# Kernel tuning notes

Hardware: AMD Instinct MI355X
Metric: run time of the kernel (lower is better)

## Reference

```python
import jax, jax.numpy as jnp
import numpy as np

B, T, K = 128, 1024, 24
START_TAG, END_TAG = 22, 23


def setup_inputs() -> dict:
    key = jax.random.key(0)
    k1, k2, k3 = jax.random.split(key, 3)
    scores = jax.random.normal(k1, (B, T, K, K), dtype=jnp.float32)
    targets = jax.random.randint(k2, (B, T), 0, K * K)
    # lengths must be sorted descending (pack_padded_sequence convention), >= 1
    lengths = jnp.sort(jax.random.randint(k3, (B,), 1, T + 1))[::-1]
    return {"scores": scores, "targets": targets, "lengths": lengths}


def reference(scores, targets, lengths):
    b, t_len, k, _ = scores.shape
    # gold path score: gather targets from flattened [B,T,K*K] view, mask by length
    flat = scores.reshape(b, t_len, k * k)
    scores_at_targets = jnp.take_along_axis(flat, targets[:, :, None], axis=2)[..., 0]  # [B,T]
    time_mask = jnp.arange(t_len)[None, :] < lengths[:, None]  # [B,T]
    gold_score = jnp.sum(jnp.where(time_mask, scores_at_targets, 0.0))

    # CRF forward recursion (log-sum-exp over previous tag), sequential over time.
    # t == 0: initialize with row of the <start> tag (all lengths >= 1).
    prev = scores[:, 0, START_TAG, :]  # [B,K]

    def step(prev, inp):
        s_t, m_t = inp  # s_t: [B,K,K], m_t: [B] bool (t < length)
        new = jax.scipy.special.logsumexp(s_t + prev[:, :, None], axis=1)  # [B,K]
        prev = jnp.where(m_t[:, None], new, prev)
        return prev, None

    s_rest = jnp.moveaxis(scores[:, 1:], 0, 1)  # time-major [T-1,B,K,K]
    m_rest = jnp.arange(1, t_len)[:, None] < lengths[None, :]  # [T-1,B]
    prev, _ = jax.lax.scan(step, prev, (s_rest, m_rest))

    all_paths_scores = prev[:, END_TAG].sum()
    return (all_paths_scores - gold_score) / b
```

## Files before the change

### kernel.cpp

```cpp
#include <hip/hip_runtime.h>

static constexpr int T_LEN = 1024;
static constexpr int KTAG = 24;
static constexpr int MAT = 576;
static constexpr int START_TAG = 22;
static constexpr int END_TAG = 23;
static constexpr int BATCH = 128;
static constexpr int CHUNK = 16;
static constexpr int NCHUNK = 64;

static constexpr float LOG2E = 1.4426950408889634f;
static constexpr float LN2   = 0.6931471805599453f;

typedef short  bf16x8 __attribute__((ext_vector_type(8)));
typedef float  f32x16 __attribute__((ext_vector_type(16)));

__device__ __forceinline__ float fexp2(float x) { return __builtin_amdgcn_exp2f(x); }
__device__ __forceinline__ float flog2(float x) { return __builtin_amdgcn_logf(x); }

__device__ __forceinline__ unsigned int f2bf(float x) {
  unsigned int u = __float_as_uint(x);
  u += 0x7FFFu + ((u >> 16) & 1u);
  return u >> 16;
}

__global__ __launch_bounds__(256) void chunkprod_kernel(
    const float* __restrict__ scores, const int* __restrict__ targets,
    const int* __restrict__ lengths,
    float* __restrict__ wsP, int* __restrict__ wsE, float* __restrict__ wsG)
{
  const int widx = threadIdx.x >> 6;
  const int lane = threadIdx.x & 63;
  const int i = blockIdx.x * 4 + widx;
  const int pr = i >> 1;
  const int anti = i & 1;
  const int b0i = pr >> 5;
  const int c0i = pr & 31;
  const int b = anti ? (127 - b0i) : b0i;
  const int c = anti ? (63 - c0i) : c0i;
  const int len = lengths[b];
  const int t0 = 1 + c * CHUNK;
  if (t0 >= len) return;
  const int n = min(CHUNK, len - t0);
  const int hd = lane >> 5;
  const int m = lane & 31;
  const int mc = m < KTAG ? m : KTAG - 1;
  const float* sb = scores + (size_t)b * T_LEN * MAT;

  {
    float gs = 0.f;
    if (lane < n) {
      int t = t0 + lane;
      gs = sb[(size_t)t * MAT + targets[b * T_LEN + t]];
    }
    #pragma unroll
    for (int off = 1; off < 64; off <<= 1) gs += __shfl_xor(gs, off, 64);
    if (lane == 0) wsG[b * NCHUNK + c] = gs;
  }

  int off1[8], off2[4];
  #pragma unroll
  for (int e = 0; e < 8; ++e) {
    int k = (e & 3) + 8 * (e >> 2) + 4 * hd;
    off1[e] = k * KTAG + mc;
  }
  #pragma unroll
  for (int e = 0; e < 4; ++e) {
    int k = 16 + e + 4 * hd;
    off2[e] = k * KTAG + mc;
  }

  float b0r[12], b1r[12], b2r[12], b3r[12];
  auto LOADA = [&](float (&buf)[12], int step) {
    const float* pb = sb + (size_t)(t0 + step) * MAT;
    #pragma unroll
    for (int e = 0; e < 8; ++e) buf[e] = pb[off1[e]];
    #pragma unroll
    for (int e = 0; e < 4; ++e) buf[8 + e] = pb[off2[e]];
  };

  unsigned int p[8];
  #pragma unroll
  for (int r = 0; r < 8; ++r) {
    int rlo = ((2 * r) & 3) + 8 * ((2 * r) >> 2) + 4 * hd;
    unsigned int v = 0;
    if (m == rlo)     v |= 0x3F80u;
    if (m == rlo + 1) v |= (0x3F80u << 16);
    p[r] = v;
  }

  int E = 0;

  auto STEPM = [&](const float (&buf)[12]) -> f32x16 {
    float av[12];
    #pragma unroll
    for (int q = 0; q < 12; ++q) av[q] = fexp2(buf[q] * LOG2E);
    bf16x8 a1, a2;
    #pragma unroll
    for (int e = 0; e < 8; ++e) a1[e] = (short)f2bf(av[e]);
    #pragma unroll
    for (int e = 0; e < 4; ++e) a2[e] = (short)f2bf(av[8 + e]);
    #pragma unroll
    for (int e = 4; e < 8; ++e) a2[e] = 0;
    union { unsigned int u[4]; bf16x8 v; } B1, B2;
    B1.u[0] = p[0]; B1.u[1] = p[1]; B1.u[2] = p[2]; B1.u[3] = p[3];
    B2.u[0] = p[4]; B2.u[1] = p[5]; B2.u[2] = p[6]; B2.u[3] = p[7];
    f32x16 d = {};
    d = __builtin_amdgcn_mfma_f32_32x32x16_bf16(a1, B1.v, d, 0, 0, 0);
    d = __builtin_amdgcn_mfma_f32_32x32x16_bf16(a2, B2.v, d, 0, 0, 0);
    return d;
  };

  auto CONV = [&](const f32x16& d) {
    int rb = __builtin_amdgcn_readfirstlane(__float_as_int(d[0]));
    int dd = ((rb >> 23) & 255) - 127;
    E += dd;
    float sc = __int_as_float((127 - dd) << 23);
    #pragma unroll
    for (int r = 0; r < 8; ++r)
      p[r] = (f2bf(d[2 * r + 1] * sc) << 16) | f2bf(d[2 * r] * sc);
  };

  LOADA(b0r, 0);
  LOADA(b1r, n > 1 ? 1 : 0);
  LOADA(b2r, n > 2 ? 2 : 0);
  LOADA(b3r, n > 3 ? 3 : 0);
  f32x16 z;
  int s = 0;
  for (;;) {
    z = STEPM(b0r);
    if (s + 1 >= n) break;
    CONV(z); { int t = s + 4; LOADA(b0r, t < n ? t : n - 1); }
    z = STEPM(b1r);
    if (s + 2 >= n) break;
    CONV(z); { int t = s + 5; LOADA(b1r, t < n ? t : n - 1); }
    z = STEPM(b2r);
    if (s + 3 >= n) break;
    CONV(z); { int t = s + 6; LOADA(b2r, t < n ? t : n - 1); }
    z = STEPM(b3r);
    if (s + 4 >= n) break;
    CONV(z); { int t = s + 7; LOADA(b3r, t < n ? t : n - 1); }
    s += 4;
  }

  if (m < KTAG) {
    float* dst = wsP + (size_t)(b * NCHUNK + c) * MAT + m * KTAG;
    *(float4*)(dst + 4 * hd)      = make_float4(z[0], z[1], z[2],  z[3]);
    *(float4*)(dst + 8 + 4 * hd)  = make_float4(z[4], z[5], z[6],  z[7]);
    *(float4*)(dst + 16 + 4 * hd) = make_float4(z[8], z[9], z[10], z[11]);
  }
  if (lane == 0) wsE[b * NCHUNK + c] = E;
}

__global__ __launch_bounds__(64) void chainmat_kernel(
    const float* __restrict__ scores, const int* __restrict__ targets,
    const float* __restrict__ wsP, const int* __restrict__ wsE,
    const float* __restrict__ wsG, const int* __restrict__ lengths,
    float* __restrict__ wsR)
{
  const int b = blockIdx.x;
  const int lane = threadIdx.x;
  const int hd = lane >> 5;
  const int m = lane & 31;
  const int mc = m < KTAG ? m : KTAG - 1;
  const int len = lengths[b];
  const int nc = (len + CHUNK - 2) >> 4;
  const float* sb = scores + (size_t)b * T_LEN * MAT;

  float gv = 0.f;
  if (lane < nc) gv = wsG[b * NCHUNK + lane];
  #pragma unroll
  for (int off = 1; off < 64; off <<= 1) gv += __shfl_xor(gv, off, 64);
  const float g0 = sb[targets[b * T_LEN]];

  if (nc == 0) {
    if (lane == 0) wsR[b] = sb[START_TAG * KTAG + END_TAG] - g0;
    return;
  }

  int ev = 0;
  if (lane < nc) ev = wsE[b * NCHUNK + lane];
  #pragma unroll
  for (int off = 1; off < 64; off <<= 1) ev += __shfl_xor(ev, off, 64);
  int E = ev;

  int off1[8], off2[4];
  #pragma unroll
  for (int e = 0; e < 8; ++e) {
    int k = (e & 3) + 8 * (e >> 2) + 4 * hd;
    off1[e] = k * KTAG + mc;
  }
  #pragma unroll
  for (int e = 0; e < 4; ++e) {
    int k = 16 + e + 4 * hd;
    off2[e] = k * KTAG + mc;
  }
  const float* pbase = wsP + (size_t)b * NCHUNK * MAT;

  float b0[12], b1[12];
  auto LOADP = [&](float (&buf)[12], int c) {
    const float* pb = pbase + (size_t)c * MAT;
    #pragma unroll
    for (int e = 0; e < 8; ++e) buf[e] = pb[off1[e]];
    #pragma unroll
    for (int e = 0; e < 4; ++e) buf[8 + e] = pb[off2[e]];
  };

  unsigned int p[8];
  #pragma unroll
  for (int r = 0; r < 8; ++r) {
    int rlo = ((2 * r) & 3) + 8 * ((2 * r) >> 2) + 4 * hd;
    unsigned int v = 0;
    if (m == rlo)     v |= 0x3F80u;
    if (m == rlo + 1) v |= (0x3F80u << 16);
    p[r] = v;
  }

  auto STEPP = [&](const float (&buf)[12]) -> f32x16 {
    bf16x8 a1, a2;
    #pragma unroll
    for (int e = 0; e < 8; ++e) a1[e] = (short)f2bf(buf[e]);
    #pragma unroll
    for (int e = 0; e < 4; ++e) a2[e] = (short)f2bf(buf[8 + e]);
    #pragma unroll
    for (int e = 4; e < 8; ++e) a2[e] = 0;
    union { unsigned int u[4]; bf16x8 v; } B1, B2;
    B1.u[0] = p[0]; B1.u[1] = p[1]; B1.u[2] = p[2]; B1.u[3] = p[3];
    B2.u[0] = p[4]; B2.u[1] = p[5]; B2.u[2] = p[6]; B2.u[3] = p[7];
    f32x16 d = {};
    d = __builtin_amdgcn_mfma_f32_32x32x16_bf16(a1, B1.v, d, 0, 0, 0);
    d = __builtin_amdgcn_mfma_f32_32x32x16_bf16(a2, B2.v, d, 0, 0, 0);
    return d;
  };
  auto CONVP = [&](const f32x16& d) {
    int rb = __builtin_amdgcn_readfirstlane(__float_as_int(d[0]));
    int dd = ((rb >> 23) & 255) - 127;
    E += dd;
    float sc = __int_as_float((127 - dd) << 23);
    #pragma unroll
    for (int r = 0; r < 8; ++r)
      p[r] = (f2bf(d[2 * r + 1] * sc) << 16) | f2bf(d[2 * r] * sc);
  };

  LOADP(b0, 0);
  LOADP(b1, nc > 1 ? 1 : 0);
  f32x16 z;
  int c = 0;
  for (;;) {
    z = STEPP(b0);
    if (c + 1 >= nc) break;
    CONVP(z); { int t = c + 2; LOADP(b0, t < nc ? t : nc - 1); }
    z = STEPP(b1);
    if (c + 2 >= nc) break;
    CONVP(z); { int t = c + 3; LOADP(b1, t < nc ? t : nc - 1); }
    c += 2;
  }

  float tau0 = fexp2(sb[START_TAG * KTAG + mc] * LOG2E);
  float v = (hd == 1 && m < KTAG) ? z[11] * tau0 : 0.f;
  #pragma unroll
  for (int off = 1; off < 64; off <<= 1) v += __shfl_xor(v, off, 64);
  if (lane == 0) {
    float logZ = ((float)E + flog2(v)) * LN2;
    wsR[b] = logZ - gv - g0;
  }
}

__global__ __launch_bounds__(64) void sum_kernel(
    const float* __restrict__ wsR, float* __restrict__ out)
{
  const int lane = threadIdx.x;
  float v = wsR[lane] + wsR[lane + 64];
  #pragma unroll
  for (int off = 1; off < 64; off <<= 1) v += __shfl_xor(v, off, 64);
  if (lane == 0) out[0] = v * (1.0f / (float)BATCH);
}

template<int DIR>
__device__ __forceinline__ int run_chain(const float* __restrict__ base, int len, int n,
                                         volatile float* __restrict__ tau,
                                         int lane, int h, int jj)
{
  int E = 0;
  float ref = 1.0f;
  float A[12], B[12], Cb[12];
  auto LOAD = [&](float (&buf)[12], int i) {
    if (DIR == 0) {
      const float* p = base + (size_t)(1 + i) * MAT + h * 12 * KTAG + jj;
      #pragma unroll
      for (int k = 0; k < 12; ++k) buf[k] = p[k * KTAG];
    } else {
      const float4* p = (const float4*)(base + (size_t)(len - 1 - i) * MAT + jj * KTAG + h * 12);
      float4 x = p[0], y = p[1], z = p[2];
      buf[0]=x.x; buf[1]=x.y; buf[2]=x.z; buf[3]=x.w;
      buf[4]=y.x; buf[5]=y.y; buf[6]=y.z; buf[7]=y.w;
      buf[8]=z.x; buf[9]=z.y; buf[10]=z.z; buf[11]=z.w;
    }
  };
  auto STEP = [&](const float (&buf)[12]) {
    int rb = __builtin_amdgcn_readfirstlane(__float_as_int(ref));
    int d = ((rb >> 23) & 255) - 127;
    float sc = __int_as_float((127 - d) << 23);
    E += d;
    float w[12];
    #pragma unroll
    for (int k = 0; k < 12; ++k) w[k] = fexp2(buf[k] * LOG2E);
    const float4* tp = (const float4*)((const float*)&tau[h * 12]);
    float4 t0 = tp[0], t1 = tp[1], t2 = tp[2];
    float a0 = t0.x*w[0], a1 = t0.y*w[1], a2 = t0.z*w[2], a3 = t0.w*w[3];
    a0 = fmaf(t1.x, w[4],  a0); a1 = fmaf(t1.y, w[5],  a1);
    a2 = fmaf(t1.z, w[6],  a2); a3 = fmaf(t1.w, w[7],  a3);
    a0 = fmaf(t2.x, w[8],  a0); a1 = fmaf(t2.y, w[9],  a1);
    a2 = fmaf(t2.z, w[10], a2); a3 = fmaf(t2.w, w[11], a3);
    float part = (a0 + a1) + (a2 + a3);
    float tot = part + __shfl_xor(part, 32, 64);
    float tn = tot * sc;
    if (lane < KTAG) tau[lane] = tn;
    ref = tn;
  };
  if (n > 0) {
    LOAD(A, 0); LOAD(B, n > 1 ? 1 : 0); LOAD(Cb, n > 2 ? 2 : 0);
    int i = 0;
    while (i + 3 <= n) {
      STEP(A);  { int ii = i + 3; LOAD(A,  ii < n ? ii : n - 1); }
      STEP(B);  { int ii = i + 4; LOAD(B,  ii < n ? ii : n - 1); }
      STEP(Cb); { int ii = i + 5; LOAD(Cb, ii < n ? ii : n - 1); }
      i += 3;
    }
    if (i < n)     STEP(A);
    if (i + 1 < n) STEP(B);
  }
  return E;
}

__global__ __launch_bounds__(128) void crf_fb_kernel(
    const float* __restrict__ scores, const int* __restrict__ lengths,
    float* __restrict__ acc)
{
  __shared__ float sm[2][32];
  __shared__ int smE[2];
  const int b = blockIdx.x;
  const int tid = threadIdx.x;
  const int wid = tid >> 6;
  const int lane = tid & 63;
  const int h = lane >> 5;
  const int j = lane & 31;
  const int jj = j < KTAG ? j : KTAG - 1;
  const int len = lengths[b];
  const float* base = scores + (size_t)b * T_LEN * MAT;
  const int m = len >> 1;
  volatile float* tau = sm[wid];
  int E;
  if (wid == 0) {
    if (lane < KTAG) tau[lane] = fexp2(base[START_TAG * KTAG + lane] * LOG2E);
    E = run_chain<0>(base, len, m, tau, lane, h, jj);
  } else {
    if (lane < KTAG) tau[lane] = (lane == END_TAG) ? 1.0f : 0.0f;
    E = run_chain<1>(base, len, len - 1 - m, tau, lane, h, jj);
  }
  if (lane == 0) smE[wid] = E;
  __syncthreads();
  if (wid == 0) {
    float v = (lane < KTAG) ? sm[0][lane] * sm[1][lane] : 0.0f;
    #pragma unroll
    for (int off = 1; off < 32; off <<= 1) v += __shfl_xor(v, off, 64);
    if (lane == 0) {
      float res = ((float)(smE[0] + smE[1]) + flog2(v)) * LN2;
      atomicAdd(acc, res);
    }
  }
}

__global__ __launch_bounds__(256) void gold_kernel(
    const float* __restrict__ scores, const int* __restrict__ targets,
    const int* __restrict__ lengths, float* __restrict__ acc)
{
  const int idx = blockIdx.x * blockDim.x + threadIdx.x;
  const int b = idx >> 10;
  const int t = idx & (T_LEN - 1);
  float v = 0.f;
  if (t < lengths[b]) v = scores[(size_t)idx * MAT + targets[idx]];
  #pragma unroll
  for (int off = 1; off < 64; off <<= 1) v += __shfl_xor(v, off, 64);
  if ((threadIdx.x & 63) == 0) atomicAdd(acc, -v);
}

__global__ void finalize_kernel(const float* __restrict__ acc, float* __restrict__ out) {
  out[0] = acc[0] * (1.0f / (float)BATCH);
}

extern "C" void kernel_launch(void* const* d_in, const int* in_sizes, int n_in,
                              void* d_out, int out_size, void* d_ws, size_t ws_size,
                              hipStream_t stream) {
  const float* scores = (const float*)d_in[0];
  const int* targets  = (const int*)d_in[1];
  const int* lengths  = (const int*)d_in[2];
  float* out = (float*)d_out;

  const size_t pbytes = (size_t)BATCH * NCHUNK * MAT * sizeof(float);
  const size_t ebytes = (size_t)BATCH * NCHUNK * sizeof(int);
  const size_t gbytes = (size_t)BATCH * NCHUNK * sizeof(float);
  const size_t need = pbytes + ebytes + gbytes + BATCH * sizeof(float);

  if (ws_size >= need) {
    float* wsP = (float*)d_ws;
    int*   wsE = (int*)((char*)d_ws + pbytes);
    float* wsG = (float*)((char*)d_ws + pbytes + ebytes);
    float* wsR = (float*)((char*)d_ws + pbytes + ebytes + gbytes);
    chunkprod_kernel<<<BATCH * NCHUNK / 4, 256, 0, stream>>>(scores, targets, lengths,
                                                             wsP, wsE, wsG);
    chainmat_kernel<<<BATCH, 64, 0, stream>>>(scores, targets, wsP, wsE, wsG,
                                              lengths, wsR);
    sum_kernel<<<1, 64, 0, stream>>>(wsR, out);
  } else {
    float* acc = (float*)d_ws;
    hipMemsetAsync(acc, 0, sizeof(float), stream);
    gold_kernel<<<BATCH * T_LEN / 256, 256, 0, stream>>>(scores, targets, lengths, acc);
    crf_fb_kernel<<<BATCH, 128, 0, stream>>>(scores, lengths, acc);
    finalize_kernel<<<1, 1, 0, stream>>>(acc, out);
  }
}
```

Measured before the change: 66.21 us.

## Stage score tiles via async global-to-LDS loads and double chunk length

After: 60.25 us. -9.0%, faster.

```diff
diff --git a/kernel.cpp b/kernel.cpp
--- a/kernel.cpp
+++ b/kernel.cpp
@@ -6,14 +6,17 @@
 static constexpr int START_TAG = 22;
 static constexpr int END_TAG = 23;
 static constexpr int BATCH = 128;
-static constexpr int CHUNK = 16;
-static constexpr int NCHUNK = 64;
+static constexpr int CHUNK = 32;
+static constexpr int NCHUNK = 32;
 
 static constexpr float LOG2E = 1.4426950408889634f;
 static constexpr float LN2   = 0.6931471805599453f;
 
 typedef short  bf16x8 __attribute__((ext_vector_type(8)));
 typedef float  f32x16 __attribute__((ext_vector_type(16)));
+
+typedef const __attribute__((address_space(1))) void* gas_t;
+typedef __attribute__((address_space(3))) void* las_t;
 
 __device__ __forceinline__ float fexp2(float x) { return __builtin_amdgcn_exp2f(x); }
 __device__ __forceinline__ float flog2(float x) { return __builtin_amdgcn_logf(x); }
@@ -29,15 +32,16 @@
     const int* __restrict__ lengths,
     float* __restrict__ wsP, int* __restrict__ wsE, float* __restrict__ wsG)
 {
+  __shared__ float stage[4][4][576];
   const int widx = threadIdx.x >> 6;
   const int lane = threadIdx.x & 63;
   const int i = blockIdx.x * 4 + widx;
   const int pr = i >> 1;
   const int anti = i & 1;
-  const int b0i = pr >> 5;
-  const int c0i = pr & 31;
+  const int b0i = pr >> 4;
+  const int c0i = pr & 15;
   const int b = anti ? (127 - b0i) : b0i;
-  const int c = anti ? (63 - c0i) : c0i;
+  const int c = anti ? (31 - c0i) : c0i;
   const int len = lengths[b];
   const int t0 = 1 + c * CHUNK;
   if (t0 >= len) return;
@@ -57,6 +61,7 @@
     for (int off = 1; off < 64; off <<= 1) gs += __shfl_xor(gs, off, 64);
     if (lane == 0) wsG[b * NCHUNK + c] = gs;
   }
+  asm volatile("s_waitcnt vmcnt(0)" ::: "memory");
 
   int off1[8], off2[4];
   #pragma unroll
@@ -70,13 +75,12 @@
     off2[e] = k * KTAG + mc;
   }
 
-  float b0r[12], b1r[12], b2r[12], b3r[12];
-  auto LOADA = [&](float (&buf)[12], int step) {
-    const float* pb = sb + (size_t)(t0 + step) * MAT;
-    #pragma unroll
-    for (int e = 0; e < 8; ++e) buf[e] = pb[off1[e]];
-    #pragma unroll
-    for (int e = 0; e < 4; ++e) buf[8 + e] = pb[off2[e]];
+  auto STAGE = [&](int slot, int t) {
+    const float* src = sb + (size_t)(t0 + t) * MAT;
+    float* dst = &stage[widx][slot][0];
+    __builtin_amdgcn_global_load_lds((gas_t)(src + lane * 4),       (las_t)dst,        16, 0, 0);
+    __builtin_amdgcn_global_load_lds((gas_t)(src + 256 + lane * 4), (las_t)(dst + 256),16, 0, 0);
+    __builtin_amdgcn_global_load_lds((gas_t)(src + 512 + lane),     (las_t)(dst + 512), 4, 0, 0);
   };
 
   unsigned int p[8];
@@ -121,26 +125,27 @@
       p[r] = (f2bf(d[2 * r + 1] * sc) << 16) | f2bf(d[2 * r] * sc);
   };
 
-  LOADA(b0r, 0);
-  LOADA(b1r, n > 1 ? 1 : 0);
-  LOADA(b2r, n > 2 ? 2 : 0);
-  LOADA(b3r, n > 3 ? 3 : 0);
+  STAGE(0, 0);
+  STAGE(1, n > 1 ? 1 : 0);
+  STAGE(2, n > 2 ? 2 : 0);
+  STAGE(3, n > 3 ? 3 : 0);
+
   f32x16 z;
   int s = 0;
   for (;;) {
-    z = STEPM(b0r);
+    asm volatile("s_waitcnt vmcnt(9)" ::: "memory");
+    const float* sl = &stage[widx][s & 3][0];
+    float raw[12];
+    #pragma unroll
+    for (int e = 0; e < 8; ++e) raw[e] = sl[off1[e]];
+    #pragma unroll
+    for (int e = 0; e < 4; ++e) raw[8 + e] = sl[off2[e]];
+    asm volatile("s_waitcnt lgkmcnt(0)" ::: "memory");
+    if (s + 1 < n) { int t = s + 4; STAGE(s & 3, t < n ? t : n - 1); }
+    z = STEPM(raw);
     if (s + 1 >= n) break;
-    CONV(z); { int t = s + 4; LOADA(b0r, t < n ? t : n - 1); }
-    z = STEPM(b1r);
-    if (s + 2 >= n) break;
-    CONV(z); { int t = s + 5; LOADA(b1r, t < n ? t : n - 1); }
-    z = STEPM(b2r);
-    if (s + 3 >= n) break;
-    CONV(z); { int t = s + 6; LOADA(b2r, t < n ? t : n - 1); }
-    z = STEPM(b3r);
-    if (s + 4 >= n) break;
-    CONV(z); { int t = s + 7; LOADA(b3r, t < n ? t : n - 1); }
-    s += 4;
+    CONV(z);
+    ++s;
   }
 
   if (m < KTAG) {
@@ -164,7 +169,7 @@
   const int m = lane & 31;
   const int mc = m < KTAG ? m : KTAG - 1;
   const int len = lengths[b];
-  const int nc = (len + CHUNK - 2) >> 4;
+  const int nc = (len + 30) >> 5;
   const float* sb = scores + (size_t)b * T_LEN * MAT;
 
   float gv = 0.f;
```

## Double chunk length, renormalize every other step, fuse final sum via atomic counter

Applied to the files above, without the earlier changes.

Result: faster. 61.79 us (-6.7%).

```diff
diff --git a/kernel.cpp b/kernel.cpp
--- a/kernel.cpp
+++ b/kernel.cpp
@@ -6,8 +6,8 @@
 static constexpr int START_TAG = 22;
 static constexpr int END_TAG = 23;
 static constexpr int BATCH = 128;
-static constexpr int CHUNK = 16;
-static constexpr int NCHUNK = 64;
+static constexpr int CHUNK = 32;
+static constexpr int NCHUNK = 32;
 
 static constexpr float LOG2E = 1.4426950408889634f;
 static constexpr float LN2   = 0.6931471805599453f;
@@ -34,10 +34,10 @@
   const int i = blockIdx.x * 4 + widx;
   const int pr = i >> 1;
   const int anti = i & 1;
-  const int b0i = pr >> 5;
-  const int c0i = pr & 31;
+  const int b0i = pr >> 4;
+  const int c0i = pr & 15;
   const int b = anti ? (127 - b0i) : b0i;
-  const int c = anti ? (63 - c0i) : c0i;
+  const int c = anti ? (31 - c0i) : c0i;
   const int len = lengths[b];
   const int t0 = 1 + c * CHUNK;
   if (t0 >= len) return;
@@ -111,7 +111,12 @@
     return d;
   };
 
-  auto CONV = [&](const f32x16& d) {
+  auto CONVL = [&](const f32x16& d) {
+    #pragma unroll
+    for (int r = 0; r < 8; ++r)
+      p[r] = (f2bf(d[2 * r + 1]) << 16) | f2bf(d[2 * r]);
+  };
+  auto CONVF = [&](const f32x16& d) {
     int rb = __builtin_amdgcn_readfirstlane(__float_as_int(d[0]));
     int dd = ((rb >> 23) & 255) - 127;
     E += dd;
@@ -130,16 +135,16 @@
   for (;;) {
     z = STEPM(b0r);
     if (s + 1 >= n) break;
-    CONV(z); { int t = s + 4; LOADA(b0r, t < n ? t : n - 1); }
+    CONVL(z); { int t = s + 4; LOADA(b0r, t < n ? t : n - 1); }
     z = STEPM(b1r);
     if (s + 2 >= n) break;
-    CONV(z); { int t = s + 5; LOADA(b1r, t < n ? t : n - 1); }
+    CONVF(z); { int t = s + 5; LOADA(b1r, t < n ? t : n - 1); }
     z = STEPM(b2r);
     if (s + 3 >= n) break;
-    CONV(z); { int t = s + 6; LOADA(b2r, t < n ? t : n - 1); }
+    CONVL(z); { int t = s + 6; LOADA(b2r, t < n ? t : n - 1); }
     z = STEPM(b3r);
     if (s + 4 >= n) break;
-    CONV(z); { int t = s + 7; LOADA(b3r, t < n ? t : n - 1); }
+    CONVF(z); { int t = s + 7; LOADA(b3r, t < n ? t : n - 1); }
     s += 4;
   }
 
@@ -156,7 +161,7 @@
     const float* __restrict__ scores, const int* __restrict__ targets,
     const float* __restrict__ wsP, const int* __restrict__ wsE,
     const float* __restrict__ wsG, const int* __restrict__ lengths,
-    float* __restrict__ wsR)
+    float* __restrict__ wsR, int* __restrict__ cnt, float* __restrict__ out)
 {
   const int b = blockIdx.x;
   const int lane = threadIdx.x;
@@ -164,112 +169,113 @@
   const int m = lane & 31;
   const int mc = m < KTAG ? m : KTAG - 1;
   const int len = lengths[b];
-  const int nc = (len + CHUNK - 2) >> 4;
+  const int nc = (len + 30) >> 5;
   const float* sb = scores + (size_t)b * T_LEN * MAT;
 
-  float gv = 0.f;
-  if (lane < nc) gv = wsG[b * NCHUNK + lane];
-  #pragma unroll
-  for (int off = 1; off < 64; off <<= 1) gv += __shfl_xor(gv, off, 64);
   const float g0 = sb[targets[b * T_LEN]];
 
   if (nc == 0) {
     if (lane == 0) wsR[b] = sb[START_TAG * KTAG + END_TAG] - g0;
-    return;
-  }
-
-  int ev = 0;
-  if (lane < nc) ev = wsE[b * NCHUNK + lane];
-  #pragma unroll
-  for (int off = 1; off < 64; off <<= 1) ev += __shfl_xor(ev, off, 64);
-  int E = ev;
-
-  int off1[8], off2[4];
-  #pragma unroll
-  for (int e = 0; e < 8; ++e) {
-    int k = (e & 3) + 8 * (e >> 2) + 4 * hd;
-    off1[e] = k * KTAG + mc;
-  }
-  #pragma unroll
-  for (int e = 0; e < 4; ++e) {
-    int k = 16 + e + 4 * hd;
-    off2[e] = k * KTAG + mc;
-  }
-  const float* pbase = wsP + (size_t)b * NCHUNK * MAT;
-
-  float b0[12], b1[12];
-  auto LOADP = [&](float (&buf)[12], int c) {
-    const float* pb = pbase + (size_t)c * MAT;
-    #pragma unroll
-    for (int e = 0; e < 8; ++e) buf[e] = pb[off1[e]];
-    #pragma unroll
-    for (int e = 0; e < 4; ++e) buf[8 + e] = pb[off2[e]];
-  };
-
-  unsigned int p[8];
-  #pragma unroll
-  for (int r = 0; r < 8; ++r) {
-    int rlo = ((2 * r) & 3) + 8 * ((2 * r) >> 2) + 4 * hd;
-    unsigned int v = 0;
-    if (m == rlo)     v |= 0x3F80u;
-    if (m == rlo + 1) v |= (0x3F80u << 16);
-    p[r] = v;
-  }
-
-  auto STEPP = [&](const float (&buf)[12]) -> f32x16 {
-    bf16x8 a1, a2;
-    #pragma unroll
-    for (int e = 0; e < 8; ++e) a1[e] = (short)f2bf(buf[e]);
-    #pragma unroll
-    for (int e = 0; e < 4; ++e) a2[e] = (short)f2bf(buf[8 + e]);
-    #pragma unroll
-    for (int e = 4; e < 8; ++e) a2[e] = 0;
-    union { unsigned int u[4]; bf16x8 v; } B1, B2;
-    B1.u[0] = p[0]; B1.u[1] = p[1]; B1.u[2] = p[2]; B1.u[3] = p[3];
-    B2.u[0] = p[4]; B2.u[1] = p[5]; B2.u[2] = p[6]; B2.u[3] = p[7];
-    f32x16 d = {};
-    d = __builtin_amdgcn_mfma_f32_32x32x16_bf16(a1, B1.v, d, 0, 0, 0);
-    d = __builtin_amdgcn_mfma_f32_32x32x16_bf16(a2, B2.v, d, 0, 0, 0);
-    return d;
-  };
-  auto CONVP = [&](const f32x16& d) {
-    int rb = __builtin_amdgcn_readfirstlane(__float_as_int(d[0]));
-    int dd = ((rb >> 23) & 255) - 127;
-    E += dd;
-    float sc = __int_as_float((127 - dd) << 23);
-    #pragma unroll
-    for (int r = 0; r < 8; ++r)
-      p[r] = (f2bf(d[2 * r + 1] * sc) << 16) | f2bf(d[2 * r] * sc);
-  };
-
-  LOADP(b0, 0);
-  LOADP(b1, nc > 1 ? 1 : 0);
-  f32x16 z;
-  int c = 0;
-  for (;;) {
-    z = STEPP(b0);
-    if (c + 1 >= nc) break;
-    CONVP(z); { int t = c + 2; LOADP(b0, t < nc ? t : nc - 1); }
-    z = STEPP(b1);
-    if (c + 2 >= nc) break;
-    CONVP(z); { int t = c + 3; LOADP(b1, t < nc ? t : nc - 1); }
-    c += 2;
-  }
-
-  float tau0 = fexp2(sb[START_TAG * KTAG + mc] * LOG2E);
-  float v = (hd == 1 && m < KTAG) ? z[11] * tau0 : 0.f;
-  #pragma unroll
-  for (int off = 1; off < 64; off <<= 1) v += __shfl_xor(v, off, 64);
-  if (lane == 0) {
-    float logZ = ((float)E + flog2(v)) * LN2;
-    wsR[b] = logZ - gv - g0;
-  }
-}
-
-__global__ __launch_bounds__(64) void sum_kernel(
-    const float* __restrict__ wsR, float* __restrict__ out)
-{
-  const int lane = threadIdx.x;
+  } else {
+    float gv = 0.f;
+    if (lane < nc) gv = wsG[b * NCHUNK + lane];
+    #pragma unroll
+    for (int off = 1; off < 64; off <<= 1) gv += __shfl_xor(gv, off, 64);
+
+    int ev = 0;
+    if (lane < nc) ev = wsE[b * NCHUNK + lane];
+    #pragma unroll
+    for (int off = 1; off < 64; off <<= 1) ev += __shfl_xor(ev, off, 64);
+    int E = ev;
+
+    int off1[8], off2[4];
+    #pragma unroll
+    for (int e = 0; e < 8; ++e) {
+      int k = (e & 3) + 8 * (e >> 2) + 4 * hd;
+      off1[e] = k * KTAG + mc;
+    }
+    #pragma unroll
+    for (int e = 0; e < 4; ++e) {
+      int k = 16 + e + 4 * hd;
+      off2[e] = k * KTAG + mc;
+    }
+    const float* pbase = wsP + (size_t)b * NCHUNK * MAT;
+
+    float f0[12], f1[12];
+    auto LOADP = [&](float (&buf)[12], int c) {
+      const float* pb = pbase + (size_t)c * MAT;
+      #pragma unroll
+      for (int e = 0; e < 8; ++e) buf[e] = pb[off1[e]];
+      #pragma unroll
+      for (int e = 0; e < 4; ++e) buf[8 + e] = pb[off2[e]];
+    };
+
+    unsigned int p[8];
+    #pragma unroll
+    for (int r = 0; r < 8; ++r) {
+      int rlo = ((2 * r) & 3) + 8 * ((2 * r) >> 2) + 4 * hd;
+      unsigned int v = 0;
+      if (m == rlo)     v |= 0x3F80u;
+      if (m == rlo + 1) v |= (0x3F80u << 16);
+      p[r] = v;
+    }
+
+    auto STEPP = [&](const float (&buf)[12]) -> f32x16 {
+      bf16x8 a1, a2;
+      #pragma unroll
+      for (int e = 0; e < 8; ++e) a1[e] = (short)f2bf(buf[e]);
+      #pragma unroll
+      for (int e = 0; e < 4; ++e) a2[e] = (short)f2bf(buf[8 + e]);
+      #pragma unroll
+      for (int e = 4; e < 8; ++e) a2[e] = 0;
+      union { unsigned int u[4]; bf16x8 v; } B1, B2;
+      B1.u[0] = p[0]; B1.u[1] = p[1]; B1.u[2] = p[2]; B1.u[3] = p[3];
+      B2.u[0] = p[4]; B2.u[1] = p[5]; B2.u[2] = p[6]; B2.u[3] = p[7];
+      f32x16 d = {};
+      d = __builtin_amdgcn_mfma_f32_32x32x16_bf16(a1, B1.v, d, 0, 0, 0);
+      d = __builtin_amdgcn_mfma_f32_32x32x16_bf16(a2, B2.v, d, 0, 0, 0);
+      return d;
+    };
+    auto CONVP = [&](const f32x16& d) {
+      int rb = __builtin_amdgcn_readfirstlane(__float_as_int(d[0]));
+      int dd = ((rb >> 23) & 255) - 127;
+      E += dd;
+      float sc = __int_as_float((127 - dd) << 23);
+      #pragma unroll
+      for (int r = 0; r < 8; ++r)
+        p[r] = (f2bf(d[2 * r + 1] * sc) << 16) | f2bf(d[2 * r] * sc);
+    };
+
+    LOADP(f0, 0);
+    LOADP(f1, nc > 1 ? 1 : 0);
+    f32x16 z;
+    int c = 0;
+    for (;;) {
+      z = STEPP(f0);
+      if (c + 1 >= nc) break;
+      CONVP(z); { int t = c + 2; LOADP(f0, t < nc ? t : nc - 1); }
+      z = STEPP(f1);
+      if (c + 2 >= nc) break;
+      CONVP(z); { int t = c + 3; LOADP(f1, t < nc ? t : nc - 1); }
+      c += 2;
+    }
+
+    float tau0 = fexp2(sb[START_TAG * KTAG + mc] * LOG2E);
+    float v = (hd == 1 && m < KTAG) ? z[11] * tau0 : 0.f;
+    #pragma unroll
+    for (int off = 1; off < 64; off <<= 1) v += __shfl_xor(v, off, 64);
+    if (lane == 0) {
+      float logZ = ((float)E + flog2(v)) * LN2;
+      wsR[b] = logZ - gv - g0;
+    }
+  }
+
+  __threadfence();
+  int old = 0;
+  if (lane == 0) old = atomicAdd(cnt, 1);
+  old = __shfl(old, 0, 64);
+  if (old != BATCH - 1) return;
+  __threadfence();
   float v = wsR[lane] + wsR[lane + 64];
   #pragma unroll
   for (int off = 1; off < 64; off <<= 1) v += __shfl_xor(v, off, 64);
@@ -400,18 +406,21 @@
   const size_t pbytes = (size_t)BATCH * NCHUNK * MAT * sizeof(float);
   const size_t ebytes = (size_t)BATCH * NCHUNK * sizeof(int);
   const size_t gbytes = (size_t)BATCH * NCHUNK * sizeof(float);
-  const size_t need = pbytes + ebytes + gbytes + BATCH * sizeof(float);
+  const size_t rbytes = (size_t)BATCH * sizeof(float);
+  const size_t need = pbytes + ebytes + gbytes + rbytes + 64;
 
   if (ws_size >= need) {
-    float* wsP = (float*)d_ws;
-    int*   wsE = (int*)((char*)d_ws + pbytes);
-    float* wsG = (float*)((char*)d_ws + pbytes + ebytes);
-    float* wsR = (float*)((char*)d_ws + pbytes + ebytes + gbytes);
+    char* base = (char*)d_ws;
+    float* wsP = (float*)base;
+    int*   wsE = (int*)(base + pbytes);
+    float* wsG = (float*)(base + pbytes + ebytes);
+    float* wsR = (float*)(base + pbytes + ebytes + gbytes);
+    int*   cnt = (int*)(base + pbytes + ebytes + gbytes + rbytes);
+    hipMemsetAsync(cnt, 0, 64, stream);
     chunkprod_kernel<<<BATCH * NCHUNK / 4, 256, 0, stream>>>(scores, targets, lengths,
                                                              wsP, wsE, wsG);
     chainmat_kernel<<<BATCH, 64, 0, stream>>>(scores, targets, wsP, wsE, wsG,
-                                              lengths, wsR);
-    sum_kernel<<<1, 64, 0, stream>>>(wsR, out);
+                                              lengths, wsR, cnt, out);
   } else {
     float* acc = (float*)d_ws;
     hipMemsetAsync(acc, 0, sizeof(float), stream);
```
